# Performance work log

Hardware: AMD Instinct MI355X
Metric: run time of the kernel (lower is better)

The kernel has to match this reference:

```python
import jax, jax.numpy as jnp
import numpy as np

B, T, E, HID, V, K = 32, 512, 512, 512, 50257, 12
H = HID // 2          # per-direction LSTM hidden
START, STOP = 10, 11  # tag_to_ix['<START>'], tag_to_ix['<STOP>']
NEG = -10000.0


def setup_inputs() -> dict:
    key = jax.random.key(0)
    ks = jax.random.split(key, 16)
    sentence = jax.random.randint(ks[0], (B, T), 0, V)
    embed = jax.random.normal(ks[1], (V, E), jnp.float32) * 0.1
    # torch LSTM weights, gate order (i, f, g, o); biases fused (b_ih + b_hh)
    w_ih_f = jax.random.normal(ks[2], (4 * H, E), jnp.float32) * 0.05
    w_hh_f = jax.random.normal(ks[3], (4 * H, H), jnp.float32) * 0.05
    b_f = jax.random.normal(ks[4], (4 * H,), jnp.float32) * 0.05
    w_ih_b = jax.random.normal(ks[5], (4 * H, E), jnp.float32) * 0.05
    w_hh_b = jax.random.normal(ks[6], (4 * H, H), jnp.float32) * 0.05
    b_b = jax.random.normal(ks[7], (4 * H,), jnp.float32) * 0.05
    # init_hidden(): random initial states, [2 directions, B, H]
    h0 = jax.random.normal(ks[8], (2, B, H), jnp.float32)
    c0 = jax.random.normal(ks[9], (2, B, H), jnp.float32)
    W_out = jax.random.normal(ks[10], (K, HID), jnp.float32) * 0.05
    b_out = jax.random.normal(ks[11], (K,), jnp.float32) * 0.05
    transitions = jax.random.normal(ks[12], (K, K), jnp.float32)
    transitions = transitions.at[START, :].set(NEG).at[:, STOP].set(NEG)
    return dict(sentence=sentence, embed=embed,
                w_ih_f=w_ih_f, w_hh_f=w_hh_f, b_f=b_f,
                w_ih_b=w_ih_b, w_hh_b=w_hh_b, b_b=b_b,
                h0=h0, c0=c0, W_out=W_out, b_out=b_out,
                transitions=transitions)


def _lstm_dir(x, w_ih, w_hh, b, h0, c0, reverse):
    # x: [B, T, E] -> hidden sequence [B, T, H]
    xg = jnp.einsum('bte,ge->btg', x, w_ih) + b  # [B, T, 4H] input pre-activations

    def step(carry, xt):
        h, c = carry
        g = xt + h @ w_hh.T
        i, f, gg, o = jnp.split(g, 4, axis=-1)
        c = jax.nn.sigmoid(f) * c + jax.nn.sigmoid(i) * jnp.tanh(gg)
        h = jax.nn.sigmoid(o) * jnp.tanh(c)
        return (h, c), h

    _, ys = jax.lax.scan(step, (h0, c0), jnp.swapaxes(xg, 0, 1), reverse=reverse)
    return jnp.swapaxes(ys, 0, 1)


def reference(sentence, embed, w_ih_f, w_hh_f, b_f, w_ih_b, w_hh_b, b_b,
              h0, c0, W_out, b_out, transitions):
    # _get_lstm_features
    x = embed[sentence]  # [B, T, E]
    hf = _lstm_dir(x, w_ih_f, w_hh_f, b_f, h0[0], c0[0], False)
    hb = _lstm_dir(x, w_ih_b, w_hh_b, b_b, h0[1], c0[1], True)
    feats = jnp.concatenate([hf, hb], axis=-1) @ W_out.T + b_out  # [B, T, K]

    # _viterbi_decode: fused per-timestep max/argmax recurrence
    init = jnp.full((B, K), NEG, jnp.float32).at[:, START].set(0.0)

    def vstep(fv, feat_t):
        # scores[b, next, prev] = fv[b, prev] + transitions[next, prev]
        scores = fv[:, None, :] + transitions[None, :, :]
        bptr = jnp.argmax(scores, axis=2)            # [B, K]
        fv_new = jnp.max(scores, axis=2) + feat_t     # emit score added after max
        return fv_new, bptr

    fv, bptrs = jax.lax.scan(vstep, init, jnp.swapaxes(feats, 0, 1))  # bptrs [T, B, K]
    terminal = fv + transitions[STOP]                 # [B, K]
    best = jnp.argmax(terminal, axis=1)               # [B]
    # faithful to original: terminal_var[:, best_tag_id] -> [B, B]
    path_score = jnp.take(terminal, best, axis=1)

    def back(tag, bp):
        prev = jnp.take_along_axis(bp, tag[:, None], axis=1)[:, 0]
        return prev, prev

    _, ys = jax.lax.scan(back, best, bptrs, reverse=True)  # ys[t] = tag at position t-1
    # path positions 0..T-1 are (ys[1:], best); ys[0] is START (dropped by [:,1:])
    best_path = jnp.concatenate([ys[1:], best[None, :]], axis=0).T  # [B, T]
    return path_score, best_path
```

## Files before the change

### kernel.cpp

```cpp
#include <hip/hip_runtime.h>
#include <hip/hip_bf16.h>


typedef __attribute__((ext_vector_type(8))) __bf16 bf16x8;
typedef __attribute__((ext_vector_type(8))) unsigned short u16x8;
typedef __attribute__((ext_vector_type(4))) float  f32x4;

#define MFMA16(a, b, c) __builtin_amdgcn_mfma_f32_16x16x32_bf16((a), (b), (c), 0, 0, 0)

__device__ __forceinline__ float sigm(float x) { return 1.0f / (1.0f + __expf(-x)); }
__device__ __forceinline__ float tanh_f(float x) {
  x = fminf(fmaxf(x, -15.0f), 15.0f);
  float e = __expf(2.0f * x);
  return (e - 1.0f) / (e + 1.0f);
}

__device__ __forceinline__ void split8(const float* v, bf16x8& hi, bf16x8& lo) {
#pragma unroll
  for (int j = 0; j < 8; j++) {
    __bf16 h = (__bf16)v[j];
    hi[j] = h;
    lo[j] = (__bf16)(v[j] - (float)h);
  }
}

__global__ __launch_bounds__(256) void xg_gemm(
    const int* __restrict__ sent, const float* __restrict__ embed,
    const float* __restrict__ wih_f, const float* __restrict__ wih_b,
    const float* __restrict__ bias_f, const float* __restrict__ bias_b,
    float* __restrict__ xg)
{
  __shared__ __bf16 Ah[128][40], Al[128][40];
  __shared__ __bf16 Bh[128][40], Bl[128][40];
  __shared__ int toks[128];
  const int tid = threadIdx.x;
  const int m0 = blockIdx.x * 128, n0 = blockIdx.y * 128;
  if (tid < 128) toks[tid] = sent[m0 + tid];
  const int wave = tid >> 6, lane = tid & 63, q = lane >> 4, c = lane & 15;
  const int wy = wave >> 1, wx = wave & 1;
  f32x4 acc[4][4];
  for (int mt = 0; mt < 4; mt++)
    for (int nt = 0; nt < 4; nt++)
      acc[mt][nt] = f32x4{0.0f, 0.0f, 0.0f, 0.0f};
  __syncthreads();

  for (int k0 = 0; k0 < 512; k0 += 32) {
#pragma unroll
    for (int i = 0; i < 2; i++) {
      int ch = tid + (i << 8);
      int r = ch >> 2, kc = ch & 3;
      float tmp[8];
      const float* asrc = embed + (size_t)toks[r] * 512 + k0 + kc * 8;
#pragma unroll
      for (int j = 0; j < 8; j++) tmp[j] = asrc[j];
      bf16x8 hi, lo;
      split8(tmp, hi, lo);
      *(bf16x8*)&Ah[r][kc * 8] = hi;
      *(bf16x8*)&Al[r][kc * 8] = lo;
      int n = n0 + r;
      const float* wsrc = (n < 1024) ? (wih_f + (size_t)n * 512)
                                     : (wih_b + (size_t)(n - 1024) * 512);
#pragma unroll
      for (int j = 0; j < 8; j++) tmp[j] = wsrc[k0 + kc * 8 + j];
      split8(tmp, hi, lo);
      *(bf16x8*)&Bh[r][kc * 8] = hi;
      *(bf16x8*)&Bl[r][kc * 8] = lo;
    }
    __syncthreads();
    bf16x8 ah[4], al[4], bh[4], bl[4];
#pragma unroll
    for (int t4 = 0; t4 < 4; t4++) {
      int ar = wy * 64 + t4 * 16 + c, br = wx * 64 + t4 * 16 + c;
      ah[t4] = *(const bf16x8*)&Ah[ar][q * 8];
      al[t4] = *(const bf16x8*)&Al[ar][q * 8];
      bh[t4] = *(const bf16x8*)&Bh[br][q * 8];
      bl[t4] = *(const bf16x8*)&Bl[br][q * 8];
    }
#pragma unroll
    for (int mt = 0; mt < 4; mt++)
#pragma unroll
      for (int nt = 0; nt < 4; nt++) {
        acc[mt][nt] = MFMA16(ah[mt], bh[nt], acc[mt][nt]);
        acc[mt][nt] = MFMA16(al[mt], bh[nt], acc[mt][nt]);
        acc[mt][nt] = MFMA16(ah[mt], bl[nt], acc[mt][nt]);
      }
    __syncthreads();
  }

#pragma unroll
  for (int nt = 0; nt < 4; nt++) {
    int n = n0 + wx * 64 + nt * 16 + c;
    float bval = (n < 1024) ? bias_f[n] : bias_b[n - 1024];
#pragma unroll
    for (int mt = 0; mt < 4; mt++) {
      int mbase = m0 + wy * 64 + mt * 16 + q * 4;
#pragma unroll
      for (int reg = 0; reg < 4; reg++)
        xg[(size_t)(mbase + reg) * 2048 + n] = acc[mt][nt][reg] + bval;
    }
  }
}

__global__ __launch_bounds__(256, 1) void lstm_rec(
    const float* __restrict__ xg,
    const float* __restrict__ whh_f, const float* __restrict__ whh_b,
    const float* __restrict__ h0, const float* __restrict__ c0,
    float* __restrict__ h_seq,
    unsigned int* __restrict__ hx,
    int* __restrict__ flags)
{
  const int blk = blockIdx.x;
  const int d = blk >> 2, hs = blk & 3;
  const int tid = threadIdx.x;
  const int wave = tid >> 6, lane = tid & 63, q = lane >> 4, c = lane & 15;
  const float* __restrict__ whh = d ? whh_b : whh_f;

  __shared__ __bf16 hfrag[2][2][16][512];

  bf16x8 wfh[4][8], wfl[4][8];
#pragma unroll
  for (int g = 0; g < 4; g++) {
    int row = g * 256 + hs * 64 + wave * 16 + c;
    const float* wr = whh + (size_t)row * 256;
#pragma unroll
    for (int ks = 0; ks < 8; ks++) {
      float tmp[8];
#pragma unroll
      for (int j = 0; j < 8; j++) tmp[j] = wr[ks * 32 + q * 8 + j];
      split8(tmp, wfh[g][ks], wfl[g][ks]);
    }
  }
  const int ug = hs * 64 + wave * 16 + c;
  float cst[2][4];
#pragma unroll
  for (int mt = 0; mt < 2; mt++)
#pragma unroll
    for (int reg = 0; reg < 4; reg++)
      cst[mt][reg] = c0[d * 8192 + (mt * 16 + q * 4 + reg) * 256 + ug];

  const int sb = tid >> 3;
  const int kc4 = (tid & 7) * 4;

  auto load_xv = [&](float (&xv)[2][4][4], int tt) {
#pragma unroll
    for (int mt = 0; mt < 2; mt++)
#pragma unroll
      for (int reg = 0; reg < 4; reg++) {
        int b = mt * 16 + q * 4 + reg;
        const float* xr = xg + ((size_t)(b * 512 + tt) << 11) + (d << 10) + ug;
#pragma unroll
        for (int g = 0; g < 4; g++)
          xv[mt][g][reg] = xr[g << 8];
      }
  };

  float xv_cur[2][4][4];
  load_xv(xv_cur, d ? 511 : 0);

  for (int s = 0; s < 512; s++) {
    const int t_seq = d ? (511 - s) : s;
    const int p = s & 1;

    if (s == 0) {
#pragma unroll
      for (int i = 0; i < 4; i++) {
        int kc = kc4 + i;
        float tmp[8];
        const float* src = h0 + d * 8192 + sb * 256 + kc * 8;
#pragma unroll
        for (int j = 0; j < 8; j++) tmp[j] = src[j];
        bf16x8 vhi, vlo;
        split8(tmp, vhi, vlo);
        int fid = ((sb >> 4) << 3) + (kc >> 2);
        int cid = ((kc & 3) << 4) + (sb & 15);
        int pos = cid ^ (fid & 7);
        *(bf16x8*)&hfrag[0][0][fid][pos * 8] = vhi;
        *(bf16x8*)&hfrag[0][1][fid][pos * 8] = vlo;
      }
    } else {
      const int* fp = flags + ((d * 512 + (s - 1)) << 4) + (lane & 15);
      int fv = __hip_atomic_load(fp, __ATOMIC_RELAXED, __HIP_MEMORY_SCOPE_AGENT);
      while (!__all(fv == s)) {
        __builtin_amdgcn_s_sleep(1);
        fv = __hip_atomic_load(fp, __ATOMIC_RELAXED, __HIP_MEMORY_SCOPE_AGENT);
      }

      const unsigned long long* hb64 = (const unsigned long long*)
          (hx + ((size_t)((d * 2 + p) * 32 + sb)) * 256 + kc4 * 8);
      unsigned long long v64[16];
#pragma unroll
      for (int i = 0; i < 16; i++)
        v64[i] = __hip_atomic_load(hb64 + i, __ATOMIC_RELAXED,
                                   __HIP_MEMORY_SCOPE_AGENT);
#pragma unroll
      for (int i = 0; i < 4; i++) {
        int kc = kc4 + i;
        u16x8 vhi, vlo;
#pragma unroll
        for (int j = 0; j < 8; j++) {
          unsigned long long dv = v64[i * 4 + (j >> 1)];
          unsigned int w32 = (j & 1) ? (unsigned int)(dv >> 32)
                                     : (unsigned int)dv;
          vhi[j] = (unsigned short)(w32 >> 16);
          vlo[j] = (unsigned short)(w32 & 0xffffu);
        }
        int fid = ((sb >> 4) << 3) + (kc >> 2);
        int cid = ((kc & 3) << 4) + (sb & 15);
        int pos = cid ^ (fid & 7);
        *(u16x8*)&hfrag[p][0][fid][pos * 8] = vhi;
        *(u16x8*)&hfrag[p][1][fid][pos * 8] = vlo;
      }
    }

    f32x4 acc[2][4];
#pragma unroll
    for (int mt = 0; mt < 2; mt++)
#pragma unroll
      for (int g = 0; g < 4; g++)
#pragma unroll
        for (int reg = 0; reg < 4; reg++)
          acc[mt][g][reg] = xv_cur[mt][g][reg];

    __syncthreads();

#pragma unroll
    for (int ks = 0; ks < 8; ks++) {
      int pos = (lane ^ ks) * 8;
      bf16x8 ahi0 = *(const bf16x8*)&hfrag[p][0][ks][pos];
      bf16x8 ahi1 = *(const bf16x8*)&hfrag[p][0][8 + ks][pos];
      bf16x8 alo0 = *(const bf16x8*)&hfrag[p][1][ks][pos];
      bf16x8 alo1 = *(const bf16x8*)&hfrag[p][1][8 + ks][pos];
#pragma unroll
      for (int g = 0; g < 4; g++) {
        acc[0][g] = MFMA16(ahi0, wfh[g][ks], acc[0][g]);
        acc[1][g] = MFMA16(ahi1, wfh[g][ks], acc[1][g]);
        acc[0][g] = MFMA16(alo0, wfh[g][ks], acc[0][g]);
        acc[1][g] = MFMA16(alo1, wfh[g][ks], acc[1][g]);
        acc[0][g] = MFMA16(ahi0, wfl[g][ks], acc[0][g]);
        acc[1][g] = MFMA16(ahi1, wfl[g][ks], acc[1][g]);
      }
    }

    const int pn = (s + 1) & 1;
    float hv[2][4];
#pragma unroll
    for (int mt = 0; mt < 2; mt++)
#pragma unroll
      for (int reg = 0; reg < 4; reg++) {
        int b = mt * 16 + q * 4 + reg;
        float iv = sigm(acc[mt][0][reg]);
        float fg = sigm(acc[mt][1][reg]);
        float gv = tanh_f(acc[mt][2][reg]);
        float ov = sigm(acc[mt][3][reg]);
        float cn = fg * cst[mt][reg] + iv * gv;
        cst[mt][reg] = cn;
        float hn = ov * tanh_f(cn);
        hv[mt][reg] = hn;
        __bf16 hhi = (__bf16)hn;
        __bf16 hlo = (__bf16)(hn - (float)hhi);
        unsigned int pack =
            ((unsigned int)__builtin_bit_cast(unsigned short, hhi) << 16) |
            (unsigned int)__builtin_bit_cast(unsigned short, hlo);
        __hip_atomic_store(&hx[((size_t)((d * 2 + pn) * 32 + b)) * 256 + ug], pack,
                           __ATOMIC_RELAXED, __HIP_MEMORY_SCOPE_AGENT);
      }

    asm volatile("s_waitcnt vmcnt(0)" ::: "memory");
    if (lane == 0)
      __hip_atomic_store(&flags[((d * 512 + s) << 4) + hs * 4 + wave], s + 1,
                         __ATOMIC_RELAXED, __HIP_MEMORY_SCOPE_AGENT);

#pragma unroll
    for (int mt = 0; mt < 2; mt++)
#pragma unroll
      for (int reg = 0; reg < 4; reg++) {
        int b = mt * 16 + q * 4 + reg;
        h_seq[((size_t)(b * 512 + t_seq) << 9) + (d << 8) + ug] = hv[mt][reg];
      }

    if (s < 511) {
      float xv_nxt[2][4][4];
      load_xv(xv_nxt, d ? (511 - (s + 1)) : (s + 1));
#pragma unroll
      for (int mt = 0; mt < 2; mt++)
#pragma unroll
        for (int g = 0; g < 4; g++)
#pragma unroll
          for (int reg = 0; reg < 4; reg++)
            xv_cur[mt][g][reg] = xv_nxt[mt][g][reg];
    }
  }
}

__global__ __launch_bounds__(256) void feats_k(
    const float* __restrict__ h_seq, const float* __restrict__ W_out,
    const float* __restrict__ b_out, float* __restrict__ feats)
{
  int m = blockIdx.x * 4 + (threadIdx.x >> 6);
  int lane = threadIdx.x & 63;
  const float4* hp = (const float4*)(h_seq + (size_t)m * 512 + lane * 8);
  float4 a = hp[0], b2 = hp[1];
  float h[8] = {a.x, a.y, a.z, a.w, b2.x, b2.y, b2.z, b2.w};
#pragma unroll
  for (int k = 0; k < 12; k++) {
    const float4* wp = (const float4*)(W_out + k * 512 + lane * 8);
    float4 w0 = wp[0], w1 = wp[1];
    float w[8] = {w0.x, w0.y, w0.z, w0.w, w1.x, w1.y, w1.z, w1.w};
    float p = 0.0f;
#pragma unroll
    for (int j = 0; j < 8; j++) p += h[j] * w[j];
#pragma unroll
    for (int off = 32; off > 0; off >>= 1) p += __shfl_xor(p, off);
    if (lane == 0) feats[(size_t)m * 12 + k] = p + b_out[k];
  }
}

__global__ __launch_bounds__(64) void viterbi_k(
    const float* __restrict__ feats, const float* __restrict__ trans,
    float* __restrict__ terminal, int* __restrict__ best,
    float* __restrict__ out_path)
{
  const int b = blockIdx.x;
  const int lane = threadIdx.x;
  __shared__ unsigned char bp[512][12];
  float trow[12];
#pragma unroll
  for (int pv = 0; pv < 12; pv++)
    trow[pv] = (lane < 12) ? trans[lane * 12 + pv] : -10000.0f;
  float fv = (lane == 10) ? 0.0f : -10000.0f;
  for (int t = 0; t < 512; t++) {
    float bestv = -3.4e38f;
    int arg = 0;
#pragma unroll
    for (int pv = 0; pv < 12; pv++) {
      float sc = __shfl(fv, pv) + trow[pv];
      if (sc > bestv) { bestv = sc; arg = pv; }
    }
    float ft = (lane < 12) ? feats[(size_t)(b * 512 + t) * 12 + lane] : 0.0f;
    if (lane < 12) {
      bp[t][lane] = (unsigned char)arg;
      fv = bestv + ft;
    }
  }
  float term = fv + ((lane < 12) ? trans[11 * 12 + lane] : 0.0f);
  if (lane < 12) terminal[b * 12 + lane] = term;
  float v = (lane < 12) ? term : -3.4e38f;
  int idx = lane;
#pragma unroll
  for (int off = 8; off > 0; off >>= 1) {
    float ov = __shfl_down(v, off);
    int oi = __shfl_down(idx, off);
    if (ov > v || (ov == v && oi < idx)) { v = ov; idx = oi; }
  }
  int bidx = __shfl(idx, 0);
  __syncthreads();
  if (lane == 0) {
    best[b] = bidx;
    int tag = bidx;
    out_path[b * 512 + 511] = (float)bidx;
    for (int t = 511; t >= 1; t--) {
      tag = bp[t][tag];
      out_path[b * 512 + t - 1] = (float)tag;
    }
  }
}

__global__ __launch_bounds__(256) void pscore_k(
    const float* __restrict__ terminal, const int* __restrict__ best,
    float* __restrict__ out)
{
  int idx = blockIdx.x * 256 + threadIdx.x;
  if (idx < 1024) {
    int i = idx >> 5, j = idx & 31;
    out[idx] = terminal[i * 12 + best[j]];
  }
}

extern "C" void kernel_launch(void* const* d_in, const int* in_sizes, int n_in,
                              void* d_out, int out_size, void* d_ws, size_t ws_size,
                              hipStream_t stream)
{
  const int*   sent  = (const int*)d_in[0];
  const float* embed = (const float*)d_in[1];
  const float* wih_f = (const float*)d_in[2];
  const float* whh_f = (const float*)d_in[3];
  const float* b_f   = (const float*)d_in[4];
  const float* wih_b = (const float*)d_in[5];
  const float* whh_b = (const float*)d_in[6];
  const float* b_b   = (const float*)d_in[7];
  const float* h0    = (const float*)d_in[8];
  const float* c0    = (const float*)d_in[9];
  const float* W_out = (const float*)d_in[10];
  const float* b_out = (const float*)d_in[11];
  const float* trans = (const float*)d_in[12];

  char* ws = (char*)d_ws;
  float*        xg    = (float*)(ws);
  float*        h_seq = (float*)(ws + 134217728);
  float*        feats = (float*)(ws + 167772160);
  unsigned int* hx    = (unsigned int*)(ws + 168558592);
  int*          flags = (int*)(ws + 168689664);
  float*        term  = (float*)(ws + 168755200);
  int*          best  = (int*)(ws + 168756736);

  float* outp = (float*)d_out;

  hipMemsetAsync(flags, 0, 2 * 512 * 16 * sizeof(int), stream);
  xg_gemm<<<dim3(128, 16), 256, 0, stream>>>(sent, embed, wih_f, wih_b, b_f, b_b, xg);
  lstm_rec<<<8, 256, 0, stream>>>(xg, whh_f, whh_b, h0, c0, h_seq, hx, flags);
  feats_k<<<4096, 256, 0, stream>>>(h_seq, W_out, b_out, feats);
  viterbi_k<<<32, 64, 0, stream>>>(feats, trans, term, best, outp + 1024);
  pscore_k<<<4, 256, 0, stream>>>(term, best, outp);
}
```

Measured before the change: 3.961 ms.

## Split LSTM recurrence batch into two groups with per-group flags for overlap

Each timestep of the cross-block LSTM recurrence now runs as two half-batch phases of 16 rows each. Each phase waits on its own flag set, computes, publishes its h values and signals before the next phase starts. This lets other blocks begin the first half of step s+1 while the second half of step s is still in flight, hiding inter-block synchronisation latency behind MFMA work. The cost is twice as many barriers and flag polls per step and a single-buffered shared fragment array. The flags buffer is moved inside the feats workspace region and doubled in size.

```diff
diff --git a/kernel.cpp b/kernel.cpp
--- a/kernel.cpp
+++ b/kernel.cpp
@@ -115,7 +115,7 @@
   const int wave = tid >> 6, lane = tid & 63, q = lane >> 4, c = lane & 15;
   const float* __restrict__ whh = d ? whh_b : whh_f;
 
-  __shared__ __bf16 hfrag[2][2][16][512];
+  __shared__ __bf16 hfrag[2][16][512];
 
   bf16x8 wfh[4][8], wfl[4][8];
 #pragma unroll
@@ -139,6 +139,7 @@
       cst[mt][reg] = c0[d * 8192 + (mt * 16 + q * 4 + reg) * 256 + ug];
 
   const int sb = tid >> 3;
+  const int grp = sb >> 4;
   const int kc4 = (tid & 7) * 4;
 
   auto load_xv = [&](float (&xv)[2][4][4], int tt) {
@@ -160,102 +161,97 @@
   for (int s = 0; s < 512; s++) {
     const int t_seq = d ? (511 - s) : s;
     const int p = s & 1;
-
-    if (s == 0) {
-#pragma unroll
-      for (int i = 0; i < 4; i++) {
-        int kc = kc4 + i;
-        float tmp[8];
-        const float* src = h0 + d * 8192 + sb * 256 + kc * 8;
-#pragma unroll
-        for (int j = 0; j < 8; j++) tmp[j] = src[j];
-        bf16x8 vhi, vlo;
-        split8(tmp, vhi, vlo);
-        int fid = ((sb >> 4) << 3) + (kc >> 2);
-        int cid = ((kc & 3) << 4) + (sb & 15);
-        int pos = cid ^ (fid & 7);
-        *(bf16x8*)&hfrag[0][0][fid][pos * 8] = vhi;
-        *(bf16x8*)&hfrag[0][1][fid][pos * 8] = vlo;
-      }
-    } else {
-      const int* fp = flags + ((d * 512 + (s - 1)) << 4) + (lane & 15);
-      int fv = __hip_atomic_load(fp, __ATOMIC_RELAXED, __HIP_MEMORY_SCOPE_AGENT);
-      while (!__all(fv == s)) {
-        __builtin_amdgcn_s_sleep(1);
-        fv = __hip_atomic_load(fp, __ATOMIC_RELAXED, __HIP_MEMORY_SCOPE_AGENT);
-      }
-
-      const unsigned long long* hb64 = (const unsigned long long*)
-          (hx + ((size_t)((d * 2 + p) * 32 + sb)) * 256 + kc4 * 8);
-      unsigned long long v64[16];
-#pragma unroll
-      for (int i = 0; i < 16; i++)
-        v64[i] = __hip_atomic_load(hb64 + i, __ATOMIC_RELAXED,
-                                   __HIP_MEMORY_SCOPE_AGENT);
-#pragma unroll
-      for (int i = 0; i < 4; i++) {
-        int kc = kc4 + i;
-        u16x8 vhi, vlo;
-#pragma unroll
-        for (int j = 0; j < 8; j++) {
-          unsigned long long dv = v64[i * 4 + (j >> 1)];
-          unsigned int w32 = (j & 1) ? (unsigned int)(dv >> 32)
-                                     : (unsigned int)dv;
-          vhi[j] = (unsigned short)(w32 >> 16);
-          vlo[j] = (unsigned short)(w32 & 0xffffu);
+    const int pn = (s + 1) & 1;
+
+#pragma unroll
+    for (int g = 0; g < 2; g++) {
+      if (s == 0) {
+        if (grp == g) {
+#pragma unroll
+          for (int i = 0; i < 4; i++) {
+            int kc = kc4 + i;
+            float tmp[8];
+            const float* src = h0 + d * 8192 + sb * 256 + kc * 8;
+#pragma unroll
+            for (int j = 0; j < 8; j++) tmp[j] = src[j];
+            bf16x8 vhi, vlo;
+            split8(tmp, vhi, vlo);
+            int fid = (grp << 3) + (kc >> 2);
+            int cid = ((kc & 3) << 4) + (sb & 15);
+            int pos = cid ^ (fid & 7);
+            *(bf16x8*)&hfrag[0][fid][pos * 8] = vhi;
+            *(bf16x8*)&hfrag[1][fid][pos * 8] = vlo;
+          }
         }
-        int fid = ((sb >> 4) << 3) + (kc >> 2);
-        int cid = ((kc & 3) << 4) + (sb & 15);
-        int pos = cid ^ (fid & 7);
-        *(u16x8*)&hfrag[p][0][fid][pos * 8] = vhi;
-        *(u16x8*)&hfrag[p][1][fid][pos * 8] = vlo;
-      }
-    }
-
-    f32x4 acc[2][4];
-#pragma unroll
-    for (int mt = 0; mt < 2; mt++)
-#pragma unroll
-      for (int g = 0; g < 4; g++)
+      } else if (grp == g) {
+        const int* fp = flags + (((d * 2 + g) * 512 + (s - 1)) << 4) + (lane & 15);
+        int fv = __hip_atomic_load(fp, __ATOMIC_RELAXED, __HIP_MEMORY_SCOPE_AGENT);
+        while (!__all(fv == s)) {
+          __builtin_amdgcn_s_sleep(1);
+          fv = __hip_atomic_load(fp, __ATOMIC_RELAXED, __HIP_MEMORY_SCOPE_AGENT);
+        }
+
+        const unsigned long long* hb64 = (const unsigned long long*)
+            (hx + ((size_t)((d * 2 + p) * 32 + sb)) * 256 + kc4 * 8);
+        unsigned long long v64[16];
+#pragma unroll
+        for (int i = 0; i < 16; i++)
+          v64[i] = __hip_atomic_load(hb64 + i, __ATOMIC_RELAXED,
+                                     __HIP_MEMORY_SCOPE_AGENT);
+#pragma unroll
+        for (int i = 0; i < 4; i++) {
+          int kc = kc4 + i;
+          u16x8 vhi, vlo;
+#pragma unroll
+          for (int j = 0; j < 8; j++) {
+            unsigned long long dv = v64[i * 4 + (j >> 1)];
+            unsigned int w32 = (j & 1) ? (unsigned int)(dv >> 32)
+                                       : (unsigned int)dv;
+            vhi[j] = (unsigned short)(w32 >> 16);
+            vlo[j] = (unsigned short)(w32 & 0xffffu);
+          }
+          int fid = (grp << 3) + (kc >> 2);
+          int cid = ((kc & 3) << 4) + (sb & 15);
+          int pos = cid ^ (fid & 7);
+          *(u16x8*)&hfrag[0][fid][pos * 8] = vhi;
+          *(u16x8*)&hfrag[1][fid][pos * 8] = vlo;
+        }
+      }
+
+      f32x4 acc[4];
+#pragma unroll
+      for (int gg = 0; gg < 4; gg++)
 #pragma unroll
         for (int reg = 0; reg < 4; reg++)
-          acc[mt][g][reg] = xv_cur[mt][g][reg];
-
-    __syncthreads();
-
-#pragma unroll
-    for (int ks = 0; ks < 8; ks++) {
-      int pos = (lane ^ ks) * 8;
-      bf16x8 ahi0 = *(const bf16x8*)&hfrag[p][0][ks][pos];
-      bf16x8 ahi1 = *(const bf16x8*)&hfrag[p][0][8 + ks][pos];
-      bf16x8 alo0 = *(const bf16x8*)&hfrag[p][1][ks][pos];
-      bf16x8 alo1 = *(const bf16x8*)&hfrag[p][1][8 + ks][pos];
-#pragma unroll
-      for (int g = 0; g < 4; g++) {
-        acc[0][g] = MFMA16(ahi0, wfh[g][ks], acc[0][g]);
-        acc[1][g] = MFMA16(ahi1, wfh[g][ks], acc[1][g]);
-        acc[0][g] = MFMA16(alo0, wfh[g][ks], acc[0][g]);
-        acc[1][g] = MFMA16(alo1, wfh[g][ks], acc[1][g]);
-        acc[0][g] = MFMA16(ahi0, wfl[g][ks], acc[0][g]);
-        acc[1][g] = MFMA16(ahi1, wfl[g][ks], acc[1][g]);
-      }
-    }
-
-    const int pn = (s + 1) & 1;
-    float hv[2][4];
-#pragma unroll
-    for (int mt = 0; mt < 2; mt++)
+          acc[gg][reg] = xv_cur[g][gg][reg];
+
+      __syncthreads();
+
+#pragma unroll
+      for (int ks = 0; ks < 8; ks++) {
+        int pos = (lane ^ ks) * 8;
+        bf16x8 ahi = *(const bf16x8*)&hfrag[0][g * 8 + ks][pos];
+        bf16x8 alo = *(const bf16x8*)&hfrag[1][g * 8 + ks][pos];
+#pragma unroll
+        for (int gg = 0; gg < 4; gg++) {
+          acc[gg] = MFMA16(ahi, wfh[gg][ks], acc[gg]);
+          acc[gg] = MFMA16(alo, wfh[gg][ks], acc[gg]);
+          acc[gg] = MFMA16(ahi, wfl[gg][ks], acc[gg]);
+        }
+      }
+
+      float hv[4];
 #pragma unroll
       for (int reg = 0; reg < 4; reg++) {
-        int b = mt * 16 + q * 4 + reg;
-        float iv = sigm(acc[mt][0][reg]);
-        float fg = sigm(acc[mt][1][reg]);
-        float gv = tanh_f(acc[mt][2][reg]);
-        float ov = sigm(acc[mt][3][reg]);
-        float cn = fg * cst[mt][reg] + iv * gv;
-        cst[mt][reg] = cn;
+        int b = g * 16 + q * 4 + reg;
+        float iv = sigm(acc[0][reg]);
+        float fg = sigm(acc[1][reg]);
+        float gv = tanh_f(acc[2][reg]);
+        float ov = sigm(acc[3][reg]);
+        float cn = fg * cst[g][reg] + iv * gv;
+        cst[g][reg] = cn;
         float hn = ov * tanh_f(cn);
-        hv[mt][reg] = hn;
+        hv[reg] = hn;
         __bf16 hhi = (__bf16)hn;
         __bf16 hlo = (__bf16)(hn - (float)hhi);
         unsigned int pack =
@@ -265,18 +261,17 @@
                            __ATOMIC_RELAXED, __HIP_MEMORY_SCOPE_AGENT);
       }
 
-    asm volatile("s_waitcnt vmcnt(0)" ::: "memory");
-    if (lane == 0)
-      __hip_atomic_store(&flags[((d * 512 + s) << 4) + hs * 4 + wave], s + 1,
-                         __ATOMIC_RELAXED, __HIP_MEMORY_SCOPE_AGENT);
-
-#pragma unroll
-    for (int mt = 0; mt < 2; mt++)
+      asm volatile("s_waitcnt vmcnt(0)" ::: "memory");
+      if (lane == 0)
+        __hip_atomic_store(&flags[(((d * 2 + g) * 512 + s) << 4) + hs * 4 + wave],
+                           s + 1, __ATOMIC_RELAXED, __HIP_MEMORY_SCOPE_AGENT);
+
 #pragma unroll
       for (int reg = 0; reg < 4; reg++) {
-        int b = mt * 16 + q * 4 + reg;
-        h_seq[((size_t)(b * 512 + t_seq) << 9) + (d << 8) + ug] = hv[mt][reg];
-      }
+        int b = g * 16 + q * 4 + reg;
+        h_seq[((size_t)(b * 512 + t_seq) << 9) + (d << 8) + ug] = hv[reg];
+      }
+    }
 
     if (s < 511) {
       float xv_nxt[2][4][4];
@@ -284,10 +279,10 @@
 #pragma unroll
       for (int mt = 0; mt < 2; mt++)
 #pragma unroll
-        for (int g = 0; g < 4; g++)
+        for (int gg = 0; gg < 4; gg++)
 #pragma unroll
           for (int reg = 0; reg < 4; reg++)
-            xv_cur[mt][g][reg] = xv_nxt[mt][g][reg];
+            xv_cur[mt][gg][reg] = xv_nxt[mt][gg][reg];
     }
   }
 }
@@ -398,14 +393,14 @@
   float*        xg    = (float*)(ws);
   float*        h_seq = (float*)(ws + 134217728);
   float*        feats = (float*)(ws + 167772160);
+  int*          flags = (int*)(ws + 167772160 + 262144);
   unsigned int* hx    = (unsigned int*)(ws + 168558592);
-  int*          flags = (int*)(ws + 168689664);
-  float*        term  = (float*)(ws + 168755200);
-  int*          best  = (int*)(ws + 168756736);
+  float*        term  = (float*)(ws + 168693760);
+  int*          best  = (int*)(ws + 168695296);
 
   float* outp = (float*)d_out;
 
-  hipMemsetAsync(flags, 0, 2 * 512 * 16 * sizeof(int), stream);
+  hipMemsetAsync(flags, 0, 2 * 2 * 512 * 16 * sizeof(int), stream);
   xg_gemm<<<dim3(128, 16), 256, 0, stream>>>(sent, embed, wih_f, wih_b, b_f, b_b, xg);
   lstm_rec<<<8, 256, 0, stream>>>(xg, whh_f, whh_b, h0, c0, h_seq, hx, flags);
   feats_k<<<4096, 256, 0, stream>>>(h_seq, W_out, b_out, feats);
```

Measured after the change: 4.589 ms. 15.9% more time.
